# Optimization experiments

Hardware: AMD Instinct MI355X
Metric: run time of the kernel (lower is better)

Reference implementation:

```python
import jax, jax.numpy as jnp
import numpy as np

D_MODEL = 1024
NUM_HEADS = 16


def setup_inputs() -> dict:
    key = jax.random.key(0)
    ks = jax.random.split(key, 5)
    scale = 1.0 / np.sqrt(D_MODEL)
    X = jax.random.normal(ks[0], (4, 2048, D_MODEL), dtype=jnp.float32)
    W_q = jax.random.normal(ks[1], (D_MODEL, D_MODEL), dtype=jnp.float32) * scale
    W_k = jax.random.normal(ks[2], (D_MODEL, D_MODEL), dtype=jnp.float32) * scale
    W_v = jax.random.normal(ks[3], (D_MODEL, D_MODEL), dtype=jnp.float32) * scale
    W_o = jax.random.normal(ks[4], (D_MODEL, D_MODEL), dtype=jnp.float32) * scale
    return {"X": X, "W_q": W_q, "W_k": W_k, "W_v": W_v, "W_o": W_o}


def reference(X, W_q, W_k, W_v, W_o):
    b, s, d_model = X.shape
    h = NUM_HEADS
    d_k = d_model // h
    # Linear projections (y = x @ W^T convention; W stored as [out,in] would be
    # x @ W.T, but with random weights we use x @ W — math is identical in form).
    def split_heads(y):
        return y.reshape(b, s, h, d_k).transpose(0, 2, 1, 3)  # b h s d
    q = split_heads(X @ W_q)
    k = split_heads(X @ W_k)
    v = split_heads(X @ W_v)
    scores = jnp.einsum('bhid,bhjd->bhij', q, k) / jnp.sqrt(jnp.float32(d_k))
    causal = jnp.tril(jnp.ones((s, s), dtype=bool))
    scores = jnp.where(causal[None, None], scores, jnp.float32(-jnp.inf))
    probs = jax.nn.softmax(scores, axis=-1)
    attended = jnp.einsum('bhij,bhjd->bhid', probs, v)
    out = attended.transpose(0, 2, 1, 3).reshape(b, s, d_model)
    return out @ W_o
```

## Files before the change

### kernel.cpp

```cpp
#include <hip/hip_runtime.h>

typedef __bf16 bf16;
typedef __attribute__((ext_vector_type(8))) __bf16 bf16x8;
typedef __attribute__((ext_vector_type(4))) float f32x4;
typedef __attribute__((ext_vector_type(4))) unsigned short u16x4;

#define D_MODEL 1024
#define SEQ     2048
#define NB      4
#define NH      16
#define DK      64
#define MROWS   (NB * SEQ)

#define MFMA_BF16 __builtin_amdgcn_mfma_f32_16x16x32_bf16
#define EXP2F(x) __builtin_amdgcn_exp2f(x)
#define QSCALE 0.18033688011112042f

__device__ __forceinline__ bf16 f2b(float f) {
    union { float f; unsigned u; } c; c.f = f;
    unsigned r = (c.u + 0x7fffu + ((c.u >> 16) & 1u)) >> 16;
    union { unsigned short s; bf16 b; } o; o.s = (unsigned short)r;
    return o.b;
}
__device__ __forceinline__ unsigned short f2u(float f) {
    union { float f; unsigned u; } c; c.f = f;
    return (unsigned short)((c.u + 0x7fffu + ((c.u >> 16) & 1u)) >> 16);
}
__device__ __forceinline__ unsigned fbits(float f) {
    union { float f; unsigned u; } c; c.f = f; return c.u;
}
__device__ __forceinline__ unsigned pack2(float lo, float hi) {
    return __builtin_amdgcn_perm(fbits(hi), fbits(lo), 0x07060302u);
}

__global__ void prep_kernel(const float* __restrict__ X,
                            const float* __restrict__ Wq, const float* __restrict__ Wk,
                            const float* __restrict__ Wv, const float* __restrict__ Wo,
                            bf16* __restrict__ Xb, bf16* __restrict__ WqkT,
                            bf16* __restrict__ WvT, bf16* __restrict__ WoT) {
    __shared__ float tile[32][33];
    const int bid = blockIdx.x;
    if (bid < 8192) {
        int i = bid * 256 + threadIdx.x;
        float4 v = ((const float4*)X)[i];
        u16x4 o; o[0] = f2u(v.x); o[1] = f2u(v.y); o[2] = f2u(v.z); o[3] = f2u(v.w);
        ((u16x4*)Xb)[i] = o;
    } else {
        int r = bid - 8192;
        int w = r >> 10, tl = r & 1023;
        const float* src = (w == 0) ? Wq : (w == 1) ? Wk : (w == 2) ? Wv : Wo;
        bf16* dst = (w == 0) ? WqkT : (w == 1) ? WqkT + (size_t)1024 * 1024
                  : (w == 2) ? WvT : WoT;
        const int n0 = (tl & 31) * 32, k0 = (tl >> 5) * 32;
        const int tx = threadIdx.x & 31, ty = threadIdx.x >> 5;
#pragma unroll
        for (int i = 0; i < 4; i++)
            tile[ty + i * 8][tx] = src[(size_t)(k0 + ty + i * 8) * 1024 + n0 + tx];
        __syncthreads();
#pragma unroll
        for (int i = 0; i < 4; i++)
            dst[(size_t)(n0 + ty + i * 8) * 1024 + k0 + tx] = f2b(tile[tx][ty + i * 8]);
    }
}

template <int MODE>
__global__ __launch_bounds__(256) void gemm128(const bf16* __restrict__ A,
                                               const bf16* __restrict__ Bt,
                                               void* __restrict__ out) {
    __shared__ __align__(16) bf16 lA[128 * 64];
    __shared__ __align__(16) bf16 lB[128 * 64];

    const int t = threadIdx.x;
    const int wid = t >> 6, lane = t & 63;
    const int ln = lane & 15, qd = lane >> 4;
    const int wm = wid >> 1, wn = wid & 1;
    const int row0 = blockIdx.y * 128, col0 = blockIdx.x * 128;

    const int srow = t >> 3;
    const int schunk = (t & 7) ^ (srow & 7);
    const bf16* ga = A  + (size_t)(row0 + srow) * 1024 + schunk * 8;
    const bf16* gb = Bt + (size_t)(col0 + srow) * 1024 + schunk * 8;
    const int swk = ln & 7;

    f32x4 acc[4][4];
#pragma unroll
    for (int i = 0; i < 4; i++)
#pragma unroll
        for (int j = 0; j < 4; j++) acc[i][j] = (f32x4){0.f, 0.f, 0.f, 0.f};

    for (int kb = 0; kb < 1024; kb += 64) {
#pragma unroll
        for (int c = 0; c < 4; c++) {
            __builtin_amdgcn_global_load_lds(
                (const __attribute__((address_space(1))) void*)(ga + kb + (size_t)c * 32 * 1024),
                (__attribute__((address_space(3))) void*)(&lA[t * 8 + c * 2048]), 16, 0, 0);
            __builtin_amdgcn_global_load_lds(
                (const __attribute__((address_space(1))) void*)(gb + kb + (size_t)c * 32 * 1024),
                (__attribute__((address_space(3))) void*)(&lB[t * 8 + c * 2048]), 16, 0, 0);
        }
        __syncthreads();

#pragma unroll
        for (int ks = 0; ks < 2; ks++) {
            bf16x8 af[4], bfr[4];
#pragma unroll
            for (int i = 0; i < 4; i++)
                af[i] = *(const bf16x8*)&lA[(wm * 64 + i * 16 + ln) * 64
                                            + ((ks * 4 + qd) ^ swk) * 8];
#pragma unroll
            for (int j = 0; j < 4; j++)
                bfr[j] = *(const bf16x8*)&lB[(wn * 64 + j * 16 + ln) * 64
                                             + ((ks * 4 + qd) ^ swk) * 8];
#pragma unroll
            for (int i = 0; i < 4; i++)
#pragma unroll
                for (int j = 0; j < 4; j++) {
                    if (MODE == 2)
                        acc[i][j] = MFMA_BF16(af[i], bfr[j], acc[i][j], 0, 0, 0);
                    else
                        acc[i][j] = MFMA_BF16(bfr[j], af[i], acc[i][j], 0, 0, 0);
                }
        }
        __syncthreads();
    }

#pragma unroll
    for (int i = 0; i < 4; i++)
#pragma unroll
        for (int j = 0; j < 4; j++) {
            if (MODE == 0) {
                int m  = row0 + wm * 64 + i * 16 + ln;
                int n0 = col0 + wn * 64 + j * 16 + qd * 4;
                *(f32x4*)&((float*)out)[(size_t)m * 1024 + n0] = acc[i][j];
            } else if (MODE == 1) {
                int m  = row0 + wm * 64 + i * 16 + ln;
                int n0 = col0 + wn * 64 + j * 16 + qd * 4;
                float scale = (n0 < 1024) ? QSCALE : 1.0f;
                int b = m >> 11, s = m & 2047;
                int h = (n0 & 1023) >> 6, d0 = n0 & 63;
                size_t addr = (((size_t)(b * NH + h) * SEQ + s) * DK + d0)
                              + (size_t)(n0 >> 10) * 8388608;
                u16x4 w;
#pragma unroll
                for (int r = 0; r < 4; r++) w[r] = f2u(acc[i][j][r] * scale);
                *(u16x4*)&((bf16*)out)[addr] = w;
            } else {
                int m0 = row0 + wm * 64 + i * 16 + qd * 4;
                int n  = col0 + wn * 64 + j * 16 + ln;
                int b = m0 >> 11, s0 = m0 & 2047;
                int h = n >> 6, d = n & 63;
                size_t addr = ((size_t)(b * NH + h) * DK + d) * SEQ + s0;
                u16x4 w;
#pragma unroll
                for (int r = 0; r < 4; r++) w[r] = f2u(acc[i][j][r]);
                *(u16x4*)&((bf16*)out)[addr] = w;
            }
        }
}

__global__ __launch_bounds__(256) void attn_kernel(const bf16* __restrict__ Q,
                                                   const bf16* __restrict__ K,
                                                   const bf16* __restrict__ Vt,
                                                   bf16* __restrict__ attn_out) {
    __shared__ __align__(16) bf16 kbuf[2][64 * 64];
    __shared__ __align__(16) bf16 vbuf[2][64 * 64];
    __shared__ __align__(16) bf16 plds[4][16 * 64];

    const int t = threadIdx.x;
    const int wid = t >> 6, lane = t & 63;
    const int ln = lane & 15, qd = lane >> 4;

    const int bid = blockIdx.x;
    const int bh   = ((bid >> 7) << 3) | (bid & 7);
    const int pair = (bid >> 3) & 15;
    const int gA = pair, gB = 31 - pair;
    const int ntA = gA + 1, ntT = 33;

    const bf16* Qh = Q  + (size_t)bh * SEQ * DK;
    const bf16* Kh = K  + (size_t)bh * SEQ * DK;
    const bf16* Vh = Vt + (size_t)bh * DK * SEQ;
    bf16* pw = &plds[wid][0];

    const int srow = t >> 3;
    const int schunk = (t & 7) ^ (srow & 7);
    const bf16* kgp = Kh + (size_t)srow * DK + schunk * 8;
    const bf16* vgp = Vh + (size_t)srow * SEQ + schunk * 8;
    const int swk = ln & 7;

    f32x4 o[4];
    float l;
    int qw0;
    bf16x8 qf0, qf1;

    auto stage = [&](int kb, int buf) {
#pragma unroll
        for (int c = 0; c < 2; c++) {
            __builtin_amdgcn_global_load_lds(
                (const __attribute__((address_space(1))) void*)(kgp + (size_t)(kb + c * 32) * DK),
                (__attribute__((address_space(3))) void*)(&kbuf[buf][t * 8 + c * 2048]), 16, 0, 0);
            __builtin_amdgcn_global_load_lds(
                (const __attribute__((address_space(1))) void*)(vgp + (size_t)c * 32 * SEQ + kb),
                (__attribute__((address_space(3))) void*)(&vbuf[buf][t * 8 + c * 2048]), 16, 0, 0);
        }
    };
    auto initGroup = [&](int g) {
        qw0 = g * 64 + wid * 16;
        qf0 = *(const bf16x8*)(Qh + (size_t)(qw0 + ln) * DK + qd * 8);
        qf1 = *(const bf16x8*)(Qh + (size_t)(qw0 + ln) * DK + 32 + qd * 8);
#pragma unroll
        for (int c = 0; c < 4; c++) o[c] = (f32x4){0.f, 0.f, 0.f, 0.f};
        l = 0.f;
    };
    const int b = bh >> 4, h = bh & 15;
    auto finalize = [&]() {
        float ll = l;
        ll += __shfl_xor(ll, 16);
        ll += __shfl_xor(ll, 32);
        float inv = 1.0f / ll;
        size_t orow = ((size_t)(b * SEQ + qw0 + ln)) * D_MODEL + h * DK;
#pragma unroll
        for (int c = 0; c < 4; c++) {
            u16x4 w;
#pragma unroll
            for (int r = 0; r < 4; r++) w[r] = f2u(o[c][r] * inv);
            *(u16x4*)&attn_out[orow + c * 16 + qd * 4] = w;
        }
    };

    stage(0, 0);
    initGroup(gA);
    int cur = 0;

    for (int i = 0; i < ntT; i++) {
        __syncthreads();
        int nx = i + 1;
        if (nx < ntT) {
            int kbn = ((nx < ntA) ? nx : nx - ntA) * 64;
            stage(kbn, cur ^ 1);
        }
        const int kb = ((i < ntA) ? i : i - ntA) * 64;
        const int nkk = min(4, max(0, ((qw0 + 15 - kb) >> 4) + 1));

        if (nkk > 0) {
            f32x4 st[4];
#pragma unroll
            for (int kk = 0; kk < 4; kk++)
                if (kk < nkk) {
                    const bf16* base = &kbuf[cur][(kk * 16 + ln) * 64];
                    bf16x8 kf0 = *(const bf16x8*)(base + ((qd    ) ^ swk) * 8);
                    bf16x8 kf1 = *(const bf16x8*)(base + ((qd + 4) ^ swk) * 8);
                    f32x4 z = (f32x4){0.f, 0.f, 0.f, 0.f};
                    st[kk] = MFMA_BF16(kf0, qf0, z, 0, 0, 0);
                    st[kk] = MFMA_BF16(kf1, qf1, st[kk], 0, 0, 0);
                }

            float ps = 0.f;
#pragma unroll
            for (int kk = 0; kk < 4; kk++) {
                unsigned pk0 = 0, pk1 = 0;
                if (kk < nkk) {
                    f32x4 s = st[kk];
                    if (kb + kk * 16 == qw0) {
#pragma unroll
                        for (int r = 0; r < 4; r++)
                            if (qd * 4 + r > ln) s[r] = -INFINITY;
                    }
                    float p0 = EXP2F(s[0]);
                    float p1 = EXP2F(s[1]);
                    float p2 = EXP2F(s[2]);
                    float p3 = EXP2F(s[3]);
                    ps += (p0 + p1) + (p2 + p3);
                    pk0 = pack2(p0, p1);
                    pk1 = pack2(p2, p3);
                }
                int cw = 2 * kk + (qd >> 1);
                *(uint2*)&pw[ln * 64 + (cw ^ swk) * 8 + (qd & 1) * 4] =
                    make_uint2(pk0, pk1);
            }
            l += ps;

            asm volatile("s_waitcnt lgkmcnt(0)" ::: "memory");

#pragma unroll
            for (int half = 0; half < 2; half++)
                if (half == 0 || nkk > 2) {
                    bf16x8 pa = *(const bf16x8*)&pw[ln * 64 + ((half * 4 + qd) ^ swk) * 8];
#pragma unroll
                    for (int c = 0; c < 4; c++) {
                        bf16x8 vf = *(const bf16x8*)&vbuf[cur][(c * 16 + ln) * 64
                                        + ((half * 4 + qd) ^ swk) * 8];
                        o[c] = MFMA_BF16(vf, pa, o[c], 0, 0, 0);
                    }
                }
        }

        if (i == ntA - 1) { finalize(); initGroup(gB); }
        cur ^= 1;
    }
    finalize();
}

extern "C" void kernel_launch(void* const* d_in, const int* in_sizes, int n_in,
                              void* d_out, int out_size, void* d_ws, size_t ws_size,
                              hipStream_t stream) {
    const float* X  = (const float*)d_in[0];
    const float* Wq = (const float*)d_in[1];
    const float* Wk = (const float*)d_in[2];
    const float* Wv = (const float*)d_in[3];
    const float* Wo = (const float*)d_in[4];
    float* out = (float*)d_out;
    char* ws = (char*)d_ws;

    bf16* Xb    = (bf16*)(ws);
    bf16* WqkT  = (bf16*)(ws + (16u << 20));
    bf16* WvT   = (bf16*)(ws + (20u << 20));
    bf16* WoT   = (bf16*)(ws + (22u << 20));
    bf16* Qb    = (bf16*)(ws + (24u << 20));
    bf16* Vt    = (bf16*)(ws + (56u << 20));
    bf16* Attn  = Xb;
    bf16* Kb    = Qb + (size_t)8388608;

    prep_kernel<<<dim3(12288), dim3(256), 0, stream>>>(X, Wq, Wk, Wv, Wo,
                                                       Xb, WqkT, WvT, WoT);

    gemm128<1><<<dim3(16, 64), dim3(256), 0, stream>>>(Xb, WqkT, Qb);
    gemm128<2><<<dim3(8, 64), dim3(256), 0, stream>>>(Xb, WvT, Vt);

    attn_kernel<<<dim3(1024), dim3(256), 0, stream>>>(Qb, Kb, Vt, Attn);

    gemm128<0><<<dim3(8, 64), dim3(256), 0, stream>>>(Attn, WoT, out);
}
```

Measured before the change: 260.8 us.

## Process two query fragments per wave in attention and remap GEMM block order

The attention kernel now gives each wave 32 query rows, two 16-row fragments, instead of 16. Each K/V tile loaded into LDS therefore feeds twice the MFMA work, and the grid halves to 512 blocks with 128-row query groups paired for causal balance. The GEMMs switch to a 1D grid with an explicit block-to-tile mapping; for the QK projection, adjacent blocks cover Q and K columns of the same rows. The attention change trades fewer blocks and more registers and LDS per wave for less K/V reload and fewer barriers per unit of work.

```diff
diff --git a/kernel.cpp b/kernel.cpp
--- a/kernel.cpp
+++ b/kernel.cpp
@@ -74,7 +74,18 @@
     const int wid = t >> 6, lane = t & 63;
     const int ln = lane & 15, qd = lane >> 4;
     const int wm = wid >> 1, wn = wid & 1;
-    const int row0 = blockIdx.y * 128, col0 = blockIdx.x * 128;
+
+    const int bid = blockIdx.x;
+    int rowb, colb;
+    if (MODE == 1) {
+        int s = bid >> 3;
+        colb = (bid & 7) * 2 + (s & 1);
+        rowb = s >> 1;
+    } else {
+        colb = bid & 7;
+        rowb = bid >> 3;
+    }
+    const int row0 = rowb * 128, col0 = colb * 128;
 
     const int srow = t >> 3;
     const int schunk = (t & 7) ^ (srow & 7);
@@ -164,22 +175,23 @@
                                                    bf16* __restrict__ attn_out) {
     __shared__ __align__(16) bf16 kbuf[2][64 * 64];
     __shared__ __align__(16) bf16 vbuf[2][64 * 64];
-    __shared__ __align__(16) bf16 plds[4][16 * 64];
+    __shared__ __align__(16) bf16 plds[4][2][16 * 64];
 
     const int t = threadIdx.x;
     const int wid = t >> 6, lane = t & 63;
     const int ln = lane & 15, qd = lane >> 4;
 
     const int bid = blockIdx.x;
-    const int bh   = ((bid >> 7) << 3) | (bid & 7);
-    const int pair = (bid >> 3) & 15;
-    const int gA = pair, gB = 31 - pair;
-    const int ntA = gA + 1, ntT = 33;
+    const int bh   = ((bid >> 6) << 3) | (bid & 7);
+    const int pair = (bid >> 3) & 7;
+    const int gA = pair, gB = 15 - pair;
+    const int ntA = 2 * gA + 2, ntT = 36;
 
     const bf16* Qh = Q  + (size_t)bh * SEQ * DK;
     const bf16* Kh = K  + (size_t)bh * SEQ * DK;
     const bf16* Vh = Vt + (size_t)bh * DK * SEQ;
-    bf16* pw = &plds[wid][0];
+    bf16* pw0 = &plds[wid][0][0];
+    bf16* pw1 = &plds[wid][1][0];
 
     const int srow = t >> 3;
     const int schunk = (t & 7) ^ (srow & 7);
@@ -187,10 +199,10 @@
     const bf16* vgp = Vh + (size_t)srow * SEQ + schunk * 8;
     const int swk = ln & 7;
 
-    f32x4 o[4];
-    float l;
+    f32x4 o0[4], o1[4];
+    float l0, l1;
     int qw0;
-    bf16x8 qf0, qf1;
+    bf16x8 qf00, qf01, qf10, qf11;
 
     auto stage = [&](int kb, int buf) {
 #pragma unroll
@@ -204,26 +216,35 @@
         }
     };
     auto initGroup = [&](int g) {
-        qw0 = g * 64 + wid * 16;
-        qf0 = *(const bf16x8*)(Qh + (size_t)(qw0 + ln) * DK + qd * 8);
-        qf1 = *(const bf16x8*)(Qh + (size_t)(qw0 + ln) * DK + 32 + qd * 8);
-#pragma unroll
-        for (int c = 0; c < 4; c++) o[c] = (f32x4){0.f, 0.f, 0.f, 0.f};
-        l = 0.f;
+        qw0 = g * 128 + wid * 32;
+        qf00 = *(const bf16x8*)(Qh + (size_t)(qw0 + ln) * DK + qd * 8);
+        qf01 = *(const bf16x8*)(Qh + (size_t)(qw0 + ln) * DK + 32 + qd * 8);
+        qf10 = *(const bf16x8*)(Qh + (size_t)(qw0 + 16 + ln) * DK + qd * 8);
+        qf11 = *(const bf16x8*)(Qh + (size_t)(qw0 + 16 + ln) * DK + 32 + qd * 8);
+#pragma unroll
+        for (int c = 0; c < 4; c++) {
+            o0[c] = (f32x4){0.f, 0.f, 0.f, 0.f};
+            o1[c] = (f32x4){0.f, 0.f, 0.f, 0.f};
+        }
+        l0 = 0.f; l1 = 0.f;
     };
     const int b = bh >> 4, h = bh & 15;
     auto finalize = [&]() {
-        float ll = l;
-        ll += __shfl_xor(ll, 16);
-        ll += __shfl_xor(ll, 32);
-        float inv = 1.0f / ll;
-        size_t orow = ((size_t)(b * SEQ + qw0 + ln)) * D_MODEL + h * DK;
-#pragma unroll
-        for (int c = 0; c < 4; c++) {
-            u16x4 w;
-#pragma unroll
-            for (int r = 0; r < 4; r++) w[r] = f2u(o[c][r] * inv);
-            *(u16x4*)&attn_out[orow + c * 16 + qd * 4] = w;
+#pragma unroll
+        for (int f = 0; f < 2; f++) {
+            float ll = f ? l1 : l0;
+            ll += __shfl_xor(ll, 16);
+            ll += __shfl_xor(ll, 32);
+            float inv = 1.0f / ll;
+            size_t orow = ((size_t)(b * SEQ + qw0 + f * 16 + ln)) * D_MODEL + h * DK;
+#pragma unroll
+            for (int c = 0; c < 4; c++) {
+                u16x4 w;
+#pragma unroll
+                for (int r = 0; r < 4; r++)
+                    w[r] = f2u((f ? o1[c][r] : o0[c][r]) * inv);
+                *(u16x4*)&attn_out[orow + c * 16 + qd * 4] = w;
+            }
         }
     };
 
@@ -239,57 +260,75 @@
             stage(kbn, cur ^ 1);
         }
         const int kb = ((i < ntA) ? i : i - ntA) * 64;
-        const int nkk = min(4, max(0, ((qw0 + 15 - kb) >> 4) + 1));
-
-        if (nkk > 0) {
-            f32x4 st[4];
+        const int nkk1 = min(4, max(0, ((qw0 + 31 - kb) >> 4) + 1));
+        const int nkk0 = min(4, max(0, ((qw0 + 15 - kb) >> 4) + 1));
+
+        if (nkk1 > 0) {
+            f32x4 st0[4], st1[4];
 #pragma unroll
             for (int kk = 0; kk < 4; kk++)
-                if (kk < nkk) {
+                if (kk < nkk1) {
                     const bf16* base = &kbuf[cur][(kk * 16 + ln) * 64];
                     bf16x8 kf0 = *(const bf16x8*)(base + ((qd    ) ^ swk) * 8);
                     bf16x8 kf1 = *(const bf16x8*)(base + ((qd + 4) ^ swk) * 8);
                     f32x4 z = (f32x4){0.f, 0.f, 0.f, 0.f};
-                    st[kk] = MFMA_BF16(kf0, qf0, z, 0, 0, 0);
-                    st[kk] = MFMA_BF16(kf1, qf1, st[kk], 0, 0, 0);
-                }
-
-            float ps = 0.f;
+                    st1[kk] = MFMA_BF16(kf0, qf10, z, 0, 0, 0);
+                    st1[kk] = MFMA_BF16(kf1, qf11, st1[kk], 0, 0, 0);
+                    if (kk < nkk0) {
+                        st0[kk] = MFMA_BF16(kf0, qf00, z, 0, 0, 0);
+                        st0[kk] = MFMA_BF16(kf1, qf01, st0[kk], 0, 0, 0);
+                    }
+                }
+
+            float ps0 = 0.f, ps1 = 0.f;
 #pragma unroll
             for (int kk = 0; kk < 4; kk++) {
-                unsigned pk0 = 0, pk1 = 0;
-                if (kk < nkk) {
-                    f32x4 s = st[kk];
-                    if (kb + kk * 16 == qw0) {
+                unsigned a0 = 0, a1 = 0;
+                if (kk < nkk1) {
+                    f32x4 s = st1[kk];
+                    if (kb + kk * 16 == qw0 + 16) {
 #pragma unroll
                         for (int r = 0; r < 4; r++)
                             if (qd * 4 + r > ln) s[r] = -INFINITY;
                     }
-                    float p0 = EXP2F(s[0]);
-                    float p1 = EXP2F(s[1]);
-                    float p2 = EXP2F(s[2]);
-                    float p3 = EXP2F(s[3]);
-                    ps += (p0 + p1) + (p2 + p3);
-                    pk0 = pack2(p0, p1);
-                    pk1 = pack2(p2, p3);
-                }
-                int cw = 2 * kk + (qd >> 1);
-                *(uint2*)&pw[ln * 64 + (cw ^ swk) * 8 + (qd & 1) * 4] =
-                    make_uint2(pk0, pk1);
+                    float p0 = EXP2F(s[0]), p1 = EXP2F(s[1]);
+                    float p2 = EXP2F(s[2]), p3 = EXP2F(s[3]);
+                    ps1 += (p0 + p1) + (p2 + p3);
+                    a0 = pack2(p0, p1); a1 = pack2(p2, p3);
+                }
+                int cw = (2 * kk + (qd >> 1)) ^ swk;
+                *(uint2*)&pw1[ln * 64 + cw * 8 + (qd & 1) * 4] = make_uint2(a0, a1);
+                unsigned b0 = 0, b1 = 0;
+                if (kk < nkk0) {
+                    f32x4 s = st0[kk];
+                    if (kb + kk * 16 == qw0) {
+#pragma unroll
+                        for (int r = 0; r < 4; r++)
+                            if (qd * 4 + r > ln) s[r] = -INFINITY;
+                    }
+                    float p0 = EXP2F(s[0]), p1 = EXP2F(s[1]);
+                    float p2 = EXP2F(s[2]), p3 = EXP2F(s[3]);
+                    ps0 += (p0 + p1) + (p2 + p3);
+                    b0 = pack2(p0, p1); b1 = pack2(p2, p3);
+                }
+                *(uint2*)&pw0[ln * 64 + cw * 8 + (qd & 1) * 4] = make_uint2(b0, b1);
             }
-            l += ps;
+            l1 += ps1; l0 += ps0;
 
             asm volatile("s_waitcnt lgkmcnt(0)" ::: "memory");
 
 #pragma unroll
             for (int half = 0; half < 2; half++)
-                if (half == 0 || nkk > 2) {
-                    bf16x8 pa = *(const bf16x8*)&pw[ln * 64 + ((half * 4 + qd) ^ swk) * 8];
+                if (half == 0 || nkk1 > 2) {
+                    const int pc = ((half * 4 + qd) ^ swk) * 8;
+                    bf16x8 pa1 = *(const bf16x8*)&pw1[ln * 64 + pc];
+                    bf16x8 pa0 = *(const bf16x8*)&pw0[ln * 64 + pc];
+                    bool f0act = (half == 0) ? (nkk0 > 0) : (nkk0 > 2);
 #pragma unroll
                     for (int c = 0; c < 4; c++) {
-                        bf16x8 vf = *(const bf16x8*)&vbuf[cur][(c * 16 + ln) * 64
-                                        + ((half * 4 + qd) ^ swk) * 8];
-                        o[c] = MFMA_BF16(vf, pa, o[c], 0, 0, 0);
+                        bf16x8 vf = *(const bf16x8*)&vbuf[cur][(c * 16 + ln) * 64 + pc];
+                        o1[c] = MFMA_BF16(vf, pa1, o1[c], 0, 0, 0);
+                        if (f0act) o0[c] = MFMA_BF16(vf, pa0, o0[c], 0, 0, 0);
                     }
                 }
         }
@@ -323,10 +362,10 @@
     prep_kernel<<<dim3(12288), dim3(256), 0, stream>>>(X, Wq, Wk, Wv, Wo,
                                                        Xb, WqkT, WvT, WoT);
 
-    gemm128<1><<<dim3(16, 64), dim3(256), 0, stream>>>(Xb, WqkT, Qb);
-    gemm128<2><<<dim3(8, 64), dim3(256), 0, stream>>>(Xb, WvT, Vt);
-
-    attn_kernel<<<dim3(1024), dim3(256), 0, stream>>>(Qb, Kb, Vt, Attn);
-
-    gemm128<0><<<dim3(8, 64), dim3(256), 0, stream>>>(Attn, WoT, out);
-}
+    gemm128<1><<<dim3(1024), dim3(256), 0, stream>>>(Xb, WqkT, Qb);
+    gemm128<2><<<dim3(512), dim3(256), 0, stream>>>(Xb, WvT, Vt);
+
+    attn_kernel<<<dim3(512), dim3(256), 0, stream>>>(Qb, Kb, Vt, Attn);
+
+    gemm128<0><<<dim3(512), dim3(256), 0, stream>>>(Attn, WoT, out);
+}
```

After: 272.3 us. 1.04x slower.
